# Kernel tuning notes

Measured on AMD Instinct MI355X. Metric: run time of the kernel, lower is better.

## Reference

```python
import jax, jax.numpy as jnp
import numpy as np

HIDDEN = 1280
NUM_HEADS = 16
NUM_KV_HEADS = 4
HEAD_DIM = 80
Q_SIZE = NUM_HEADS * HEAD_DIM          # 1280
KV_SIZE = NUM_KV_HEADS * HEAD_DIM      # 320
QKV_OUT = Q_SIZE + 2 * KV_SIZE         # 1920
R_SOFTPLUS_0 = 1.442695041


def setup_inputs() -> dict:
    key = jax.random.key(0)
    ks = jax.random.split(key, 6)
    B, S = 4, 2048
    return {
        "hidden_states": jax.random.normal(ks[0], (B, S, HIDDEN), dtype=jnp.float32),
        "scaling": jax.random.normal(ks[1], (HEAD_DIM,), dtype=jnp.float32),
        "qkv_w": jax.random.normal(ks[2], (QKV_OUT, HIDDEN), dtype=jnp.float32) * (1.0 / np.sqrt(HIDDEN)),
        "qkv_b": jax.random.normal(ks[3], (QKV_OUT,), dtype=jnp.float32) * 0.01,
        "o_w": jax.random.normal(ks[4], (HIDDEN, Q_SIZE), dtype=jnp.float32) * (1.0 / np.sqrt(Q_SIZE)),
        "o_b": jax.random.normal(ks[5], (HIDDEN,), dtype=jnp.float32) * 0.01,
    }


def reference(hidden_states, scaling, qkv_w, qkv_b, o_w, o_b):
    B, S, _ = hidden_states.shape
    qkv = hidden_states @ qkv_w.T + qkv_b                      # [B,S,1920]
    xq = qkv[..., :Q_SIZE].reshape(B, S, NUM_HEADS, HEAD_DIM)
    xk = qkv[..., Q_SIZE:Q_SIZE + KV_SIZE].reshape(B, S, NUM_KV_HEADS, HEAD_DIM)
    xv = qkv[..., Q_SIZE + KV_SIZE:].reshape(B, S, NUM_KV_HEADS, HEAD_DIM)
    # learned per-head-dim scaling: (r_softplus_0/sqrt(d)) * softplus(scaling)
    scale = (R_SOFTPLUS_0 / np.sqrt(HEAD_DIM)) * jax.nn.softplus(scaling)
    xq = xq * scale[None, None, None, :]
    # GQA: expand kv heads to match query heads (repeat_interleave on head dim)
    nq_per_kv = NUM_HEADS // NUM_KV_HEADS
    k = jnp.repeat(xk, nq_per_kv, axis=2)                      # [B,S,H,d]
    v = jnp.repeat(xv, nq_per_kv, axis=2)
    scores = jnp.einsum("bqhd,bkhd->bhqk", xq, k)              # [B,H,S,S]
    probs = jax.nn.softmax(scores.astype(jnp.float32), axis=-1).astype(xq.dtype)
    out = jnp.einsum("bhqk,bkhd->bqhd", probs, v)              # [B,S,H,d]
    out = out.reshape(B, S, Q_SIZE)
    return out @ o_w.T + o_b
```

## Files before the change

kernel.cpp:

```cpp
#include <hip/hip_runtime.h>

#define HIDDEN 1280
#define QOUT   1920
#define QSIZE  1280
#define KVSIZE 320
#define NHEAD  16
#define NKV    4
#define DH     80
#define SEQ    2048
#define BATCH  4
#define MTOT   (BATCH * SEQ)
#define NT64   (SEQ / 64)
#define KTILE_ELEMS 6144
#define VTILE_ELEMS 5760

typedef __attribute__((ext_vector_type(8))) short bf16x8;
typedef __attribute__((ext_vector_type(4))) short bf16x4;
typedef __attribute__((ext_vector_type(4))) float f32x4;

__device__ __forceinline__ unsigned short f2bf(float x) {
  union { float f; unsigned u; } v; v.f = x;
  unsigned r = v.u + 0x7fffu + ((v.u >> 16) & 1u);
  return (unsigned short)(r >> 16);
}

__device__ __forceinline__ unsigned packbf(float a, float b) {
  union { float f; unsigned u; } ua, ub;
  ua.f = a; ub.f = b;
  return __builtin_amdgcn_perm(ub.u + 0x8000u, ua.u + 0x8000u, 0x07060302u);
}

__device__ __forceinline__ unsigned packbf_t(float a, float b) {
  union { float f; unsigned u; } ua, ub;
  ua.f = a; ub.f = b;
  return __builtin_amdgcn_perm(ub.u, ua.u, 0x07060302u);
}

__device__ __forceinline__ float exp2x(float x) {
#if __has_builtin(__builtin_amdgcn_exp2f)
  return __builtin_amdgcn_exp2f(x);
#else
  return exp2f(x);
#endif
}

__device__ __forceinline__ void async_copy16(const void* g, void* lds) {
  __builtin_amdgcn_global_load_lds(
      (const __attribute__((address_space(1))) unsigned int*)g,
      (__attribute__((address_space(3))) unsigned int*)lds, 16, 0, 0);
}

#define HSB   (MTOT * HIDDEN / 4 / 256)
#define QWB   (QOUT * HIDDEN / 4 / 256)
#define OWB   (HIDDEN * QSIZE / 4 / 256)
__global__ __launch_bounds__(256) void prep_k(const float* __restrict__ hs,
                                              const float* __restrict__ qkv_w,
                                              const float* __restrict__ o_w,
                                              const float* __restrict__ scaling,
                                              unsigned short* __restrict__ hs_bf,
                                              unsigned short* __restrict__ qkvw_bf,
                                              unsigned short* __restrict__ ow_bf,
                                              float* __restrict__ cs) {
  const int bid = blockIdx.x, tid = threadIdx.x;
  const float* src; unsigned short* dst; int i;
  if (bid < HSB)            { src = hs;    dst = hs_bf;   i = bid * 256 + tid; }
  else if (bid < HSB + QWB) { src = qkv_w; dst = qkvw_bf; i = (bid - HSB) * 256 + tid; }
  else if (bid < HSB + QWB + OWB) { src = o_w; dst = ow_bf; i = (bid - HSB - QWB) * 256 + tid; }
  else {
    int n = (bid - HSB - QWB - OWB) * 256 + tid;
    if (n < QOUT) {
      float v = 1.0f;
      if (n < QSIZE) {
        float x = scaling[n % DH];
        float sp = (x > 20.f) ? x : log1pf(__expf(x));
        v = 1.442695041f * 1.442695041f * 0.11180339887f * sp;
      }
      cs[n] = v;
    }
    return;
  }
  float4 v = ((const float4*)src)[i];
  ushort4 o;
  o.x = f2bf(v.x); o.y = f2bf(v.y); o.z = f2bf(v.z); o.w = f2bf(v.w);
  ((ushort4*)dst)[i] = o;
}

template <bool OUT_BF16, bool USE_SCALE>
__global__ __launch_bounds__(512) void gemm_bt(const unsigned short* __restrict__ A,
                                               const unsigned short* __restrict__ Bt,
                                               const float* __restrict__ bias,
                                               const float* __restrict__ colscale,
                                               void* __restrict__ Cout,
                                               int M, int N, int K) {
  __shared__ unsigned short As[256 * 64];
  __shared__ unsigned short Bs[128 * 64];
  const int tid  = threadIdx.x;
  const int wave = tid >> 6, lane = tid & 63;
  const int r = lane & 15, quad = lane >> 4;
  const int xm = r & 7;
  const int m0 = blockIdx.y * 256, n0 = blockIdx.x * 128;
  const int rm = (wave >> 1) * 64, cn = (wave & 1) * 64;

  f32x4 acc[4][4];
#pragma unroll
  for (int i = 0; i < 4; ++i)
#pragma unroll
    for (int j = 0; j < 4; ++j) acc[i][j] = f32x4{0.f, 0.f, 0.f, 0.f};

  for (int k0 = 0; k0 < K; k0 += 64) {
    __syncthreads();
#pragma unroll
    for (int j = 0; j < 4; ++j) {
      const int c = tid + j * 512;
      const int row = c >> 3, sp = c & 7;
      const int sd = (sp ^ (row & 7)) * 8;
      async_copy16(A + (size_t)(m0 + row) * K + k0 + sd, &As[c * 8]);
    }
#pragma unroll
    for (int j = 0; j < 2; ++j) {
      const int c = tid + j * 512;
      const int row = c >> 3, sp = c & 7;
      const int sd = (sp ^ (row & 7)) * 8;
      async_copy16(Bt + (size_t)(n0 + row) * K + k0 + sd, &Bs[c * 8]);
    }
    __syncthreads();
#pragma unroll
    for (int kk = 0; kk < 2; ++kk) {
      bf16x8 af[4], bfr[4];
#pragma unroll
      for (int mi = 0; mi < 4; ++mi)
        af[mi] = *(const bf16x8*)&As[(rm + mi * 16 + r) * 64 + ((kk * 4 + quad) ^ xm) * 8];
#pragma unroll
      for (int ni = 0; ni < 4; ++ni)
        bfr[ni] = *(const bf16x8*)&Bs[(cn + ni * 16 + r) * 64 + ((kk * 4 + quad) ^ xm) * 8];
#pragma unroll
      for (int mi = 0; mi < 4; ++mi)
#pragma unroll
        for (int ni = 0; ni < 4; ++ni)
          acc[mi][ni] = __builtin_amdgcn_mfma_f32_16x16x32_bf16(af[mi], bfr[ni], acc[mi][ni], 0, 0, 0);
    }
  }

#pragma unroll
  for (int ni = 0; ni < 4; ++ni) {
    const int n = n0 + cn + ni * 16 + r;
    const float bn = bias[n];
    const float sc = USE_SCALE ? colscale[n] : 1.0f;
#pragma unroll
    for (int mi = 0; mi < 4; ++mi) {
#pragma unroll
      for (int reg = 0; reg < 4; ++reg) {
        const int m = m0 + rm + mi * 16 + quad * 4 + reg;
        const float v = (acc[mi][ni][reg] + bn) * sc;
        if (OUT_BF16)
          ((unsigned short*)Cout)[(size_t)m * N + n] = f2bf(v);
        else
          ((float*)Cout)[(size_t)m * N + n] = v;
      }
    }
  }
}

__global__ __launch_bounds__(256) void kvpack(const unsigned short* __restrict__ qkv,
                                              unsigned short* __restrict__ Kp,
                                              unsigned short* __restrict__ Vp) {
  const int st = blockIdx.x, kvh = blockIdx.y, b = blockIdx.z;
  const int tid = threadIdx.x;
  unsigned short* kout = Kp + (size_t)((b * NKV + kvh) * NT64 + st) * KTILE_ELEMS;
#pragma unroll
  for (int j = 0; j < 3; ++j) {
    int c = tid + j * 256;
    int row = c / 12, cir = c - row * 12;
    int kk = cir >> 2, sp = cir & 3;
    int sd = sp ^ ((row >> 1) & 3);
    int d0 = kk * 32 + sd * 8;
    uint4 v = {0, 0, 0, 0};
    if (d0 < DH)
      v = *(const uint4*)&qkv[(size_t)(b * SEQ + st * 64 + row) * QOUT +
                              QSIZE + kvh * DH + d0];
    *(uint4*)&kout[row * 96 + kk * 32 + sp * 8] = v;
  }
  __shared__ unsigned short tile[64][88];
  for (int c = tid; c < 640; c += 256) {
    int row = c / 10, seg = c % 10;
    uint4 v = *(const uint4*)&qkv[(size_t)(b * SEQ + st * 64 + row) * QOUT +
                                  QSIZE + KVSIZE + kvh * DH + seg * 8];
    *(uint4*)&tile[row][seg * 8] = v;
  }
  __syncthreads();
  unsigned short* vout = Vp + (size_t)((b * NKV + kvh) * NT64 + st) * VTILE_ELEMS;
  for (int c = tid; c < 5120; c += 256) {
    int d = c >> 6, key = c & 63;
    vout[d * 72 + key] = tile[key][d];
  }
}

__global__ __launch_bounds__(256, 2) void attn(const unsigned short* __restrict__ qkv,
                                               const unsigned short* __restrict__ Kp,
                                               const unsigned short* __restrict__ Vp,
                                               unsigned short* __restrict__ att) {
  const int qt = blockIdx.x, h = blockIdx.y, b = blockIdx.z;
  const int kvh = h >> 2;
  const int tid = threadIdx.x;
  const int wave = tid >> 6, lane = tid & 63;
  const int r = lane & 15, quad = lane >> 4;
  const int sq8 = (quad ^ ((r >> 1) & 3)) * 8;

  __shared__ unsigned short Ks[64 * 96];
  __shared__ unsigned short Vs[96 * 72];

  {
    const uint4 ones = {0x3F803F80u, 0x3F803F80u, 0x3F803F80u, 0x3F803F80u};
    for (int c = tid; c < 144; c += 256)
      *(uint4*)&Vs[80 * 72 + c * 8] = ones;
  }

  const int qbase = qt * 256 + wave * 64;
  bf16x8 qb[4][3];
#pragma unroll
  for (int t = 0; t < 4; ++t)
#pragma unroll
    for (int kk = 0; kk < 3; ++kk)
      qb[t][kk] = *(const bf16x8*)&qkv[(size_t)(b * SEQ + qbase + t * 16 + r) * QOUT +
                                       h * DH + kk * 32 + quad * 8];

  f32x4 o_acc[6][4];
#pragma unroll
  for (int i = 0; i < 6; ++i)
#pragma unroll
    for (int t = 0; t < 4; ++t) o_acc[i][t] = f32x4{0.f, 0.f, 0.f, 0.f};

  const unsigned short* kp = Kp + (size_t)((b * NKV + kvh) * NT64) * KTILE_ELEMS;
  const unsigned short* vp = Vp + (size_t)((b * NKV + kvh) * NT64) * VTILE_ELEMS;

  for (int kt = 0; kt < NT64; ++kt) {
    __syncthreads();
#pragma unroll
    for (int j = 0; j < 3; ++j)
      async_copy16(kp + (size_t)kt * KTILE_ELEMS + (tid + j * 256) * 8,
                   &Ks[(tid + j * 256) * 8]);
#pragma unroll
    for (int j = 0; j < 3; ++j) {
      int c = tid + j * 256;
      if (c < 720)
        async_copy16(vp + (size_t)kt * VTILE_ELEMS + c * 8, &Vs[c * 8]);
    }
    __syncthreads();

#pragma unroll
    for (int nt = 0; nt < 4; ++nt) {
      bf16x8 ka[3];
#pragma unroll
      for (int kk = 0; kk < 3; ++kk)
        ka[kk] = *(const bf16x8*)&Ks[(nt * 16 + r) * 96 + kk * 32 + sq8];

      f32x4 s[4];
#pragma unroll
      for (int t = 0; t < 4; ++t) {
        s[t] = f32x4{0.f, 0.f, 0.f, 0.f};
#pragma unroll
        for (int kk = 0; kk < 3; ++kk)
          s[t] = __builtin_amdgcn_mfma_f32_16x16x32_bf16(ka[kk], qb[t][kk], s[t], 0, 0, 0);
      }

      bf16x4 pb[4];
#pragma unroll
      for (int t = 0; t < 4; ++t) {
        union { uint2 u; bf16x4 v; } cv;
        cv.u.x = packbf_t(exp2x(s[t][0]), exp2x(s[t][1]));
        cv.u.y = packbf_t(exp2x(s[t][2]), exp2x(s[t][3]));
        pb[t] = cv.v;
      }

#pragma unroll
      for (int nt2 = 0; nt2 < 6; ++nt2) {
        union { uint2 u; bf16x4 v; } va;
        va.u = *(const uint2*)&Vs[(nt2 * 16 + r) * 72 + nt * 16 + quad * 4];
#pragma unroll
        for (int t = 0; t < 4; ++t)
          o_acc[nt2][t] = __builtin_amdgcn_mfma_f32_16x16x16bf16_1k(va.v, pb[t], o_acc[nt2][t], 0, 0, 0);
      }
    }
  }

#pragma unroll
  for (int t = 0; t < 4; ++t) {
    const float il = 1.0f / o_acc[5][t][0];
    const size_t q = (size_t)(b * SEQ + qbase + t * 16 + r);
#pragma unroll
    for (int nt2 = 0; nt2 < 5; ++nt2) {
      uint2 w;
      w.x = packbf(o_acc[nt2][t][0] * il, o_acc[nt2][t][1] * il);
      w.y = packbf(o_acc[nt2][t][2] * il, o_acc[nt2][t][3] * il);
      *(uint2*)&att[q * QSIZE + h * DH + nt2 * 16 + quad * 4] = w;
    }
  }
}

extern "C" void kernel_launch(void* const* d_in, const int* in_sizes, int n_in,
                              void* d_out, int out_size, void* d_ws, size_t ws_size,
                              hipStream_t stream) {
  const float* hs      = (const float*)d_in[0];
  const float* scaling = (const float*)d_in[1];
  const float* qkv_w   = (const float*)d_in[2];
  const float* qkv_b   = (const float*)d_in[3];
  const float* o_w     = (const float*)d_in[4];
  const float* o_b     = (const float*)d_in[5];

  char* p = (char*)d_ws;
  unsigned short* hs_bf   = (unsigned short*)p; p += (size_t)MTOT * HIDDEN * 2;
  unsigned short* qkvw_bf = (unsigned short*)p; p += (size_t)QOUT * HIDDEN * 2;
  unsigned short* ow_bf   = (unsigned short*)p; p += (size_t)HIDDEN * QSIZE * 2;
  float* cscale           = (float*)p;          p += (size_t)QOUT * 4;
  unsigned short* qkv     = (unsigned short*)p; p += (size_t)MTOT * QOUT * 2;
  unsigned short* Kp      = (unsigned short*)p; p += (size_t)BATCH * NKV * NT64 * KTILE_ELEMS * 2;
  unsigned short* Vp      = (unsigned short*)p; p += (size_t)BATCH * NKV * NT64 * VTILE_ELEMS * 2;
  unsigned short* att     = hs_bf;

  prep_k<<<HSB + QWB + OWB + 8, 256, 0, stream>>>(hs, qkv_w, o_w, scaling,
                                                  hs_bf, qkvw_bf, ow_bf, cscale);

  dim3 g1(QOUT / 128, MTOT / 256);
  gemm_bt<true, true><<<g1, 512, 0, stream>>>(hs_bf, qkvw_bf, qkv_b, cscale, qkv,
                                              MTOT, QOUT, HIDDEN);
  dim3 gp(NT64, NKV, BATCH);
  kvpack<<<gp, 256, 0, stream>>>(qkv, Kp, Vp);
  dim3 g3(SEQ / 256, NHEAD, BATCH);
  attn<<<g3, 256, 0, stream>>>(qkv, Kp, Vp, att);
  dim3 g4(QSIZE / 128, MTOT / 256);
  gemm_bt<false, false><<<g4, 512, 0, stream>>>(att, ow_bf, o_b, nullptr, d_out,
                                                MTOT, QSIZE, HIDDEN);
}
```

Measured before the change: 300.5 us.

## Use 16x16x32 MFMA for PV by permuting K rows and XOR-swizzling V tiles

The PV product now uses the K=32 bf16 MFMA instead of the K=16 variant. K rows are permuted at pack time so two score tiles combine directly into an 8-element B operand. The V tile drops its padded 72-wide layout for a 64-wide XOR-swizzled layout, which shrinks LDS traffic and avoids bank conflicts on the wider 16-byte reads. This halves the PV MFMA instruction count and the V LDS load count. The cost is more complex indexing and a larger live pw register set per pair of key tiles.

```diff
diff --git a/kernel.cpp b/kernel.cpp
--- a/kernel.cpp
+++ b/kernel.cpp
@@ -12,7 +12,7 @@
 #define MTOT   (BATCH * SEQ)
 #define NT64   (SEQ / 64)
 #define KTILE_ELEMS 6144
-#define VTILE_ELEMS 5760
+#define VTILE_ELEMS 5120
 
 typedef __attribute__((ext_vector_type(8))) short bf16x8;
 typedef __attribute__((ext_vector_type(4))) short bf16x4;
@@ -174,9 +174,10 @@
     int kk = cir >> 2, sp = cir & 3;
     int sd = sp ^ ((row >> 1) & 3);
     int d0 = kk * 32 + sd * 8;
+    int skey = (row >> 5) * 32 + ((row >> 2) & 3) * 8 + ((row >> 4) & 1) * 4 + (row & 3);
     uint4 v = {0, 0, 0, 0};
     if (d0 < DH)
-      v = *(const uint4*)&qkv[(size_t)(b * SEQ + st * 64 + row) * QOUT +
+      v = *(const uint4*)&qkv[(size_t)(b * SEQ + st * 64 + skey) * QOUT +
                               QSIZE + kvh * DH + d0];
     *(uint4*)&kout[row * 96 + kk * 32 + sp * 8] = v;
   }
@@ -191,7 +192,7 @@
   unsigned short* vout = Vp + (size_t)((b * NKV + kvh) * NT64 + st) * VTILE_ELEMS;
   for (int c = tid; c < 5120; c += 256) {
     int d = c >> 6, key = c & 63;
-    vout[d * 72 + key] = tile[key][d];
+    vout[d * 64 + (key ^ ((d & 7) << 3))] = tile[key][d];
   }
 }
 
@@ -207,12 +208,12 @@
   const int sq8 = (quad ^ ((r >> 1) & 3)) * 8;
 
   __shared__ unsigned short Ks[64 * 96];
-  __shared__ unsigned short Vs[96 * 72];
+  __shared__ unsigned short Vs[96 * 64];
 
   {
     const uint4 ones = {0x3F803F80u, 0x3F803F80u, 0x3F803F80u, 0x3F803F80u};
-    for (int c = tid; c < 144; c += 256)
-      *(uint4*)&Vs[80 * 72 + c * 8] = ones;
+    for (int c = tid; c < 128; c += 256)
+      *(uint4*)&Vs[80 * 64 + c * 8] = ones;
   }
 
   const int qbase = qt * 256 + wave * 64;
@@ -242,43 +243,54 @@
 #pragma unroll
     for (int j = 0; j < 3; ++j) {
       int c = tid + j * 256;
-      if (c < 720)
+      if (c < 640)
         async_copy16(vp + (size_t)kt * VTILE_ELEMS + c * 8, &Vs[c * 8]);
     }
     __syncthreads();
 
 #pragma unroll
-    for (int nt = 0; nt < 4; ++nt) {
-      bf16x8 ka[3];
-#pragma unroll
-      for (int kk = 0; kk < 3; ++kk)
-        ka[kk] = *(const bf16x8*)&Ks[(nt * 16 + r) * 96 + kk * 32 + sq8];
-
-      f32x4 s[4];
-#pragma unroll
-      for (int t = 0; t < 4; ++t) {
-        s[t] = f32x4{0.f, 0.f, 0.f, 0.f};
+    for (int ntp = 0; ntp < 2; ++ntp) {
+      uint4 pw[4];
+      {
+        bf16x8 ka[3];
 #pragma unroll
         for (int kk = 0; kk < 3; ++kk)
-          s[t] = __builtin_amdgcn_mfma_f32_16x16x32_bf16(ka[kk], qb[t][kk], s[t], 0, 0, 0);
-      }
-
-      bf16x4 pb[4];
-#pragma unroll
-      for (int t = 0; t < 4; ++t) {
-        union { uint2 u; bf16x4 v; } cv;
-        cv.u.x = packbf_t(exp2x(s[t][0]), exp2x(s[t][1]));
-        cv.u.y = packbf_t(exp2x(s[t][2]), exp2x(s[t][3]));
-        pb[t] = cv.v;
+          ka[kk] = *(const bf16x8*)&Ks[(ntp * 32 + r) * 96 + kk * 32 + sq8];
+#pragma unroll
+        for (int t = 0; t < 4; ++t) {
+          f32x4 s = f32x4{0.f, 0.f, 0.f, 0.f};
+#pragma unroll
+          for (int kk = 0; kk < 3; ++kk)
+            s = __builtin_amdgcn_mfma_f32_16x16x32_bf16(ka[kk], qb[t][kk], s, 0, 0, 0);
+          pw[t].x = packbf_t(exp2x(s[0]), exp2x(s[1]));
+          pw[t].y = packbf_t(exp2x(s[2]), exp2x(s[3]));
+        }
+      }
+      {
+        bf16x8 ka[3];
+#pragma unroll
+        for (int kk = 0; kk < 3; ++kk)
+          ka[kk] = *(const bf16x8*)&Ks[(ntp * 32 + 16 + r) * 96 + kk * 32 + sq8];
+#pragma unroll
+        for (int t = 0; t < 4; ++t) {
+          f32x4 s = f32x4{0.f, 0.f, 0.f, 0.f};
+#pragma unroll
+          for (int kk = 0; kk < 3; ++kk)
+            s = __builtin_amdgcn_mfma_f32_16x16x32_bf16(ka[kk], qb[t][kk], s, 0, 0, 0);
+          pw[t].z = packbf_t(exp2x(s[0]), exp2x(s[1]));
+          pw[t].w = packbf_t(exp2x(s[2]), exp2x(s[3]));
+        }
       }
 
 #pragma unroll
       for (int nt2 = 0; nt2 < 6; ++nt2) {
-        union { uint2 u; bf16x4 v; } va;
-        va.u = *(const uint2*)&Vs[(nt2 * 16 + r) * 72 + nt * 16 + quad * 4];
-#pragma unroll
-        for (int t = 0; t < 4; ++t)
-          o_acc[nt2][t] = __builtin_amdgcn_mfma_f32_16x16x16bf16_1k(va.v, pb[t], o_acc[nt2][t], 0, 0, 0);
+        bf16x8 va = *(const bf16x8*)&Vs[(nt2 * 16 + r) * 64 +
+                                        (((ntp * 4 + quad) ^ (r & 7)) << 3)];
+#pragma unroll
+        for (int t = 0; t < 4; ++t) {
+          union { uint4 u; bf16x8 v; } pv; pv.u = pw[t];
+          o_acc[nt2][t] = __builtin_amdgcn_mfma_f32_16x16x32_bf16(va, pv.v, o_acc[nt2][t], 0, 0, 0);
+        }
       }
     }
   }
```

New measurement: 283.6 us. -5.6%, faster.
